# Optimization experiments

Hardware: AMD Instinct MI355X
Metric: run time of the kernel (lower is better)

## Reference

```python
import jax, jax.numpy as jnp
import numpy as np

VS = VT = 32000; E = 512; H = 512; B = 32; S = 128; T = 128


def _gru_step(x, h, Wx, bx, Urz, brz, Un, bn):
    # x: [B, I], h: [B, H]
    gx = x @ Wx + bx                       # [B, 3H]
    xr, xz, xn = jnp.split(gx, 3, axis=-1)
    hrz = h @ Urz + brz                    # [B, 2H]
    hr, hz = jnp.split(hrz, 2, axis=-1)
    r = jax.nn.sigmoid(xr + hr)
    z = jax.nn.sigmoid(xz + hz)
    n = jnp.tanh(xn + (r * h) @ Un + bn)
    return (1.0 - z) * h + z * n


def setup_inputs() -> dict:
    key = jax.random.key(0)
    ks = jax.random.split(key, 24)
    s = 0.02
    f = lambda k, shape: (jax.random.normal(k, shape, dtype=jnp.float32) * s)
    return {
        "src": jax.random.randint(ks[0], (B, S), 0, VS),
        "tgt": jax.random.randint(ks[1], (B, T), 0, VT),
        "enc_embed": f(ks[2], (VS, E)),
        "enc_Wx": f(ks[3], (E, 3 * H)),
        "enc_bx": jnp.zeros((3 * H,), jnp.float32),
        "enc_Urz": f(ks[4], (H, 2 * H)),
        "enc_brz": jnp.zeros((2 * H,), jnp.float32),
        "enc_Un": f(ks[5], (H, H)),
        "enc_bn": jnp.zeros((H,), jnp.float32),
        "dec_embed": f(ks[6], (VT, E)),
        "dec_Wx": f(ks[7], (E + H, 3 * H)),
        "dec_bx": jnp.zeros((3 * H,), jnp.float32),
        "dec_Urz": f(ks[8], (H, 2 * H)),
        "dec_brz": jnp.zeros((2 * H,), jnp.float32),
        "dec_Un": f(ks[9], (H, H)),
        "dec_bn": jnp.zeros((H,), jnp.float32),
        "attn_Wh": f(ks[10], (H, H)),
        "attn_Ws": f(ks[11], (H, H)),
        "attn_v": f(ks[12], (H,)),
        "out_W": f(ks[13], (2 * H, VT)),
        "out_b": jnp.zeros((VT,), jnp.float32),
    }


def reference(src, tgt, enc_embed, enc_Wx, enc_bx, enc_Urz, enc_brz, enc_Un,
              enc_bn, dec_embed, dec_Wx, dec_bx, dec_Urz, dec_brz, dec_Un,
              dec_bn, attn_Wh, attn_Ws, attn_v, out_W, out_b):
    bs = src.shape[0]
    h0 = jnp.zeros((bs, H), dtype=enc_Wx.dtype)

    # -------- encoder: scan over src timesteps --------
    src_emb = enc_embed[src]                     # [B, S, E]

    def enc_step(h, x_t):
        h = _gru_step(x_t, h, enc_Wx, enc_bx, enc_Urz, enc_brz, enc_Un, enc_bn)
        return h, h

    h, enc_hs = jax.lax.scan(enc_step, h0, jnp.swapaxes(src_emb, 0, 1))
    enc_hs = jnp.swapaxes(enc_hs, 0, 1)          # [B, S, H]

    # precompute Wh(enc_hs), identical every decoder step
    wh_enc = enc_hs @ attn_Wh                    # [B, S, H]

    # -------- decoder: scan over tgt timesteps --------
    tgt_emb = dec_embed[tgt]                     # [B, T, E]

    def dec_step(h, emb_t):
        # Bahdanau attention
        energy = jnp.einsum('bsh,h->bs', jnp.tanh(wh_enc + (h @ attn_Ws)[:, None, :]), attn_v)
        attn = jax.nn.softmax(energy, axis=-1)   # [B, S]
        ctx = jnp.einsum('bs,bsh->bh', attn, enc_hs)
        x = jnp.concatenate([emb_t, ctx], axis=-1)   # [B, E+H]
        h = _gru_step(x, h, dec_Wx, dec_bx, dec_Urz, dec_brz, dec_Un, dec_bn)
        logits = jnp.concatenate([h, ctx], axis=-1) @ out_W + out_b
        out = jax.nn.log_softmax(logits, axis=-1)
        return h, out

    _, outputs = jax.lax.scan(dec_step, h, jnp.swapaxes(tgt_emb, 0, 1))
    return jnp.swapaxes(outputs, 0, 1)           # [B, T, VT]
```

## Files before the change

kernel.cpp:

```cpp
#include <hip/hip_runtime.h>
#include <stdint.h>

#define BATCH 32
#define SEQ   128
#define HID   512
#define VTOK  32000

typedef unsigned short u16;
typedef unsigned int   u32;
typedef unsigned long long u64;
typedef float    f32x4  __attribute__((ext_vector_type(4)));
typedef short    short8 __attribute__((ext_vector_type(8)));

__device__ __forceinline__ u16 f2bf(float f) {
    u32 u = __builtin_bit_cast(u32, f);
    return (u16)((u + 0x7FFFu + ((u >> 16) & 1u)) >> 16);
}
__device__ __forceinline__ float bf2f(u16 v) {
    u32 u = ((u32)v) << 16; return __builtin_bit_cast(float, u);
}
__device__ __forceinline__ float fexp2(float x) { return __builtin_amdgcn_exp2f(x); }
__device__ __forceinline__ float frcp(float x)  { return __builtin_amdgcn_rcpf(x); }
__device__ __forceinline__ float sigmoid_f(float x) {
    return frcp(1.f + fexp2(-1.442695040888963f * x));
}
__device__ __forceinline__ float tanh_f(float x) {
    return 1.f - 2.f * frcp(1.f + fexp2(2.885390081777927f * x));
}

__device__ __forceinline__ u32 ld_sc1_u32(const u32* p) {
    return __hip_atomic_load(p, __ATOMIC_RELAXED, __HIP_MEMORY_SCOPE_AGENT);
}
__device__ __forceinline__ void st_sc1_u32(u32* p, u32 v) {
    __hip_atomic_store(p, v, __ATOMIC_RELAXED, __HIP_MEMORY_SCOPE_AGENT);
}
__device__ __forceinline__ u64 ld_sc1_u64(const u64* p) {
    return __hip_atomic_load(p, __ATOMIC_RELAXED, __HIP_MEMORY_SCOPE_AGENT);
}
__device__ __forceinline__ short8 ldA(const u64* base) {
    union { u64 q[2]; short8 s; } u;
    u.q[0] = ld_sc1_u64(base);
    u.q[1] = ld_sc1_u64(base + 1);
    return u.s;
}

__device__ __forceinline__ void gbar(u32* flags, u32 gen, int nwg) {
    asm volatile("s_waitcnt vmcnt(0)" ::: "memory");
    __syncthreads();
    if (threadIdx.x == 0) st_sc1_u32(flags + (u32)blockIdx.x * 16, gen);
    const int i = threadIdx.x;
    if (i < nwg && i != (int)blockIdx.x) {
        while (ld_sc1_u32(flags + i * 16) < gen) {}
    }
    __syncthreads();
}


__global__ __launch_bounds__(256) void transpose_cvt(
    const float* __restrict__ src, u16* __restrict__ dst, int K, int N)
{
    __shared__ float tile[32][33];
    const int n0 = blockIdx.x * 32, k0 = blockIdx.y * 32;
    const int tx = threadIdx.x & 31, ty = threadIdx.x >> 5;
    #pragma unroll
    for (int j = 0; j < 32; j += 8)
        tile[ty + j][tx] = src[(size_t)(k0 + ty + j) * N + n0 + tx];
    __syncthreads();
    #pragma unroll
    for (int j = 0; j < 32; j += 8)
        dst[(size_t)(n0 + ty + j) * K + k0 + tx] = f2bf(tile[tx][ty + j]);
}

__global__ __launch_bounds__(256) void cvt_f32_bf16(
    const float* __restrict__ src, u16* __restrict__ dst)
{
    const size_t i = ((size_t)blockIdx.x * 256 + threadIdx.x) * 8;
    float4 v0 = *(const float4*)(src + i);
    float4 v1 = *(const float4*)(src + i + 4);
    uint4 pk;
    pk.x = (u32)f2bf(v0.x) | ((u32)f2bf(v0.y) << 16);
    pk.y = (u32)f2bf(v0.z) | ((u32)f2bf(v0.w) << 16);
    pk.z = (u32)f2bf(v1.x) | ((u32)f2bf(v1.y) << 16);
    pk.w = (u32)f2bf(v1.z) | ((u32)f2bf(v1.w) << 16);
    *(uint4*)(dst + i) = pk;
}

__global__ __launch_bounds__(128) void gather_emb_bf16(
    const int* __restrict__ idx, const float* __restrict__ emb, u16* __restrict__ out)
{
    const int r = blockIdx.x;
    const int token = idx[r];
    const int i = threadIdx.x * 4;
    float4 v = *(const float4*)(emb + (size_t)token * 512 + i);
    uint2 pk;
    pk.x = (u32)f2bf(v.x) | ((u32)f2bf(v.y) << 16);
    pk.y = (u32)f2bf(v.z) | ((u32)f2bf(v.w) << 16);
    *(uint2*)(out + (size_t)r * 512 + i) = pk;
}

__global__ __launch_bounds__(512) void init_state(u32* hg, u32* bar)
{
    const int i = blockIdx.x * 512 + threadIdx.x;
    hg[i] = 0u;
    if (blockIdx.x < 8) bar[blockIdx.x * 512 + threadIdx.x] = 0u;
}

__global__ __launch_bounds__(256) void gemm_bf16(
    const u16* __restrict__ A, const u16* __restrict__ BT,
    const float* __restrict__ bias, float* __restrict__ C,
    int M, int N, int K)
{
    __shared__ __align__(16) u16 As[128][40];
    __shared__ __align__(16) u16 Bs[128][40];
    const int tid  = threadIdx.x;
    const int lane = tid & 63, wave = tid >> 6;
    const int wm = (wave & 1) * 64, wn = (wave >> 1) * 64;
    const int lrow = lane & 15, lk = (lane >> 4) * 8;
    const int srow = tid >> 2, skof = (tid & 3) * 8;
    const size_t K_ = (size_t)K;
    const u16* Ag = A + ((size_t)blockIdx.y * 128 + srow) * K_ + skof;
    const u16* Bg = BT + ((size_t)blockIdx.x * 128 + srow) * K_ + skof;
    f32x4 acc[4][4] = {};
    for (int k0 = 0; k0 < K; k0 += 32) {
        uint4 a0 = *(const uint4*)(Ag + k0);
        uint4 a1 = *(const uint4*)(Ag + 64 * K_ + k0);
        uint4 b0 = *(const uint4*)(Bg + k0);
        uint4 b1 = *(const uint4*)(Bg + 64 * K_ + k0);
        __syncthreads();
        *(uint4*)&As[srow][skof]      = a0;
        *(uint4*)&As[srow + 64][skof] = a1;
        *(uint4*)&Bs[srow][skof]      = b0;
        *(uint4*)&Bs[srow + 64][skof] = b1;
        __syncthreads();
        short8 af[4], bf[4];
        #pragma unroll
        for (int i = 0; i < 4; ++i) af[i] = *(const short8*)&As[wm + i * 16 + lrow][lk];
        #pragma unroll
        for (int j = 0; j < 4; ++j) bf[j] = *(const short8*)&Bs[wn + j * 16 + lrow][lk];
        #pragma unroll
        for (int i = 0; i < 4; ++i)
            #pragma unroll
            for (int j = 0; j < 4; ++j)
                acc[i][j] = __builtin_amdgcn_mfma_f32_16x16x32_bf16(af[i], bf[j], acc[i][j], 0, 0, 0);
    }
    const int crow0 = blockIdx.y * 128 + wm + (lane >> 4) * 4;
    const int ccol0 = blockIdx.x * 128 + wn + (lane & 15);
    #pragma unroll
    for (int j = 0; j < 4; ++j) {
        const float bv = bias ? bias[ccol0 + j * 16] : 0.f;
        #pragma unroll
        for (int i = 0; i < 4; ++i)
            #pragma unroll
            for (int rr = 0; rr < 4; ++rr)
                C[(size_t)(crow0 + i * 16 + rr) * N + (ccol0 + j * 16)] = acc[i][j][rr] + bv;
    }
}

__global__ __launch_bounds__(512) void enc_coop(
    const float* __restrict__ gx, const u16* __restrict__ Urz, const u16* __restrict__ Un,
    const float* __restrict__ brz, const float* __restrict__ bn,
    u32* __restrict__ hg, u32* __restrict__ rhg, u32* __restrict__ zg,
    u16* __restrict__ enc_hs, u16* __restrict__ spack,
    u32* __restrict__ flags)
{
    const int w = blockIdx.x, tid = threadIdx.x;
    const int v = tid >> 6, lane = tid & 63;
    const int nl = lane & 15, kq = lane >> 4;
    const u64* hq = (const u64*)hg;
    const u64* rq = (const u64*)rhg;
    u32 gen = 0u;
    for (int t = 0; t < SEQ; ++t) {
        if (v < 2) {
            const int bt = v;
            const int n = w * 16 + nl;
            const int brow = bt * 16 + nl;
            float gxr_pf[4]; u32 hv_pf[4];
            #pragma unroll
            for (int rr = 0; rr < 4; ++rr) {
                const int b = bt * 16 + kq * 4 + rr;
                gxr_pf[rr] = gx[((size_t)(b * SEQ + t)) * 1536 + n];
                if (n < 512) hv_pf[rr] = ld_sc1_u32(hg + b * 256 + (n >> 1));
            }
            const u16* wp = Urz + (size_t)n * 512 + kq * 8;
            f32x4 acc = {0.f, 0.f, 0.f, 0.f};
            #pragma unroll
            for (int k0 = 0; k0 < 512; k0 += 32) {
                short8 af = ldA(hq + brow * 128 + (k0 >> 2) + kq * 2);
                short8 bf = *(const short8*)(wp + k0);
                acc = __builtin_amdgcn_mfma_f32_16x16x32_bf16(af, bf, acc, 0, 0, 0);
            }
            if (n < 512) {
                u32 pk[4];
                #pragma unroll
                for (int rr = 0; rr < 4; ++rr) {
                    const float r = sigmoid_f(gxr_pf[rr] + acc[rr] + brz[n]);
                    const float hold = bf2f((u16)((n & 1) ? (hv_pf[rr] >> 16) : (hv_pf[rr] & 0xFFFF)));
                    pk[rr] = (u32)f2bf(r * hold);
                }
                #pragma unroll
                for (int rr = 0; rr < 4; ++rr) {
                    u32 oth = (u32)__shfl_xor((int)pk[rr], 1);
                    if ((n & 1) == 0) {
                        const int b = bt * 16 + kq * 4 + rr;
                        st_sc1_u32(rhg + b * 256 + (n >> 1), (pk[rr] & 0xFFFF) | (oth << 16));
                    }
                }
            } else {
                #pragma unroll
                for (int rr = 0; rr < 4; ++rr) {
                    const int b = bt * 16 + kq * 4 + rr;
                    const float z = sigmoid_f(gxr_pf[rr] + acc[rr] + brz[n]);
                    st_sc1_u32(zg + (n - 512) * 32 + b, __float_as_uint(z));
                }
            }
        }
        gbar(flags, ++gen, 64);
        if (v < 2 && w < 32) {
            const int bt = v;
            const int n = w * 16 + nl;
            const int brow = bt * 16 + nl;
            float gxr_pf[4]; u32 hv_pf[4], zv_pf[4];
            #pragma unroll
            for (int rr = 0; rr < 4; ++rr) {
                const int b = bt * 16 + kq * 4 + rr;
                gxr_pf[rr] = gx[((size_t)(b * SEQ + t)) * 1536 + 1024 + n];
                hv_pf[rr] = ld_sc1_u32(hg + b * 256 + (n >> 1));
                zv_pf[rr] = ld_sc1_u32(zg + n * 32 + b);
            }
            const u16* wp = Un + (size_t)n * 512 + kq * 8;
            f32x4 acc = {0.f, 0.f, 0.f, 0.f};
            #pragma unroll
            for (int k0 = 0; k0 < 512; k0 += 32) {
                short8 af = ldA(rq + brow * 128 + (k0 >> 2) + kq * 2);
                short8 bf = *(const short8*)(wp + k0);
                acc = __builtin_amdgcn_mfma_f32_16x16x32_bf16(af, bf, acc, 0, 0, 0);
            }
            u32 pk[4];
            #pragma unroll
            for (int rr = 0; rr < 4; ++rr) {
                const int b = bt * 16 + kq * 4 + rr;
                const float nn = tanh_f(gxr_pf[rr] + acc[rr] + bn[n]);
                const float z = __uint_as_float(zv_pf[rr]);
                const float hold = bf2f((u16)((n & 1) ? (hv_pf[rr] >> 16) : (hv_pf[rr] & 0xFFFF)));
                const float hn = (1.f - z) * hold + z * nn;
                const u16 hb = f2bf(hn);
                pk[rr] = (u32)hb;
                enc_hs[((size_t)(b * SEQ + t)) * 512 + n] = hb;
                spack[(((size_t)b * 16 + (t >> 3)) * 512 + n) * 8 + (t & 7)] = hb;
            }
            #pragma unroll
            for (int rr = 0; rr < 4; ++rr) {
                u32 oth = (u32)__shfl_xor((int)pk[rr], 1);
                if ((n & 1) == 0) {
                    const int b = bt * 16 + kq * 4 + rr;
                    st_sc1_u32(hg + b * 256 + (n >> 1), (pk[rr] & 0xFFFF) | (oth << 16));
                }
            }
        }
        gbar(flags, ++gen, 64);
    }
}

__global__ __launch_bounds__(512) void dec_coop(
    const float* __restrict__ gxe, const u16* __restrict__ wh_bf, const u16* __restrict__ spack,
    const float* __restrict__ attn_v, const float* __restrict__ brz, const float* __restrict__ bn,
    const u16* __restrict__ Urz, const u16* __restrict__ Ws,
    const u16* __restrict__ WxC, const u16* __restrict__ Un,
    u32* __restrict__ hg, u32* __restrict__ rhg, u32* __restrict__ ctxg,
    u32* __restrict__ zg, u32* __restrict__ gg, u32* __restrict__ aWsg,
    u16* __restrict__ hctx, u32* __restrict__ flags)
{
    const int w = blockIdx.x, tid = threadIdx.x;
    const int v = tid >> 6, lane = tid & 63;
    const int nl = lane & 15, kq = lane >> 4;
    __shared__ float hWsL[4 * 132], redE[512], attnL[128];
    __shared__ u16 ctxL[512];
    const u64* hq = (const u64*)hg;
    const u64* rq = (const u64*)rhg;
    const u64* cq = (const u64*)ctxg;
    u32 gen = 0u;
    for (int t = 0; t < SEQ; ++t) {
        f32x4 aPk = {0.f, 0.f, 0.f, 0.f};
        if (v < 2) {
            const int bt = v;
            const int n = w * 16 + nl;
            const int brow = bt * 16 + nl;
            const u16* wp = (n < 1024 ? Urz + (size_t)n * 512
                                      : Ws + (size_t)(n - 1024) * 512) + kq * 8;
            f32x4 acc = {0.f, 0.f, 0.f, 0.f};
            #pragma unroll
            for (int k0 = 0; k0 < 512; k0 += 32) {
                short8 af = ldA(hq + brow * 128 + (k0 >> 2) + kq * 2);
                short8 bf = *(const short8*)(wp + k0);
                acc = __builtin_amdgcn_mfma_f32_16x16x32_bf16(af, bf, acc, 0, 0, 0);
            }
            if (n < 1024) {
                aPk = acc;
            } else {
                #pragma unroll
                for (int rr = 0; rr < 4; ++rr) {
                    const int b = bt * 16 + kq * 4 + rr;
                    st_sc1_u32(aWsg + (n - 1024) * 32 + b, __float_as_uint(acc[rr]));
                }
            }
        }
        gbar(flags, ++gen, 96);
        if (w < 32) {
            const int b = w;
            hWsL[(tid >> 7) * 132 + (tid & 127)] = __uint_as_float(ld_sc1_u32(aWsg + tid * 32 + b));
            __syncthreads();
            {
                const int s = tid >> 2, q = tid & 3;
                const u16* whr = wh_bf + ((size_t)(b * SEQ + s)) * 512 + q * 128;
                const float* avq = attn_v + q * 128;
                const float* hwq = &hWsL[q * 132];
                float e = 0.f;
                #pragma unroll 4
                for (int i = 0; i < 128; i += 8) {
                    uint4 wv = *(const uint4*)(whr + i);
                    float4 h0 = *(const float4*)(hwq + i);
                    float4 h1 = *(const float4*)(hwq + i + 4);
                    float4 v0 = *(const float4*)(avq + i);
                    float4 v1 = *(const float4*)(avq + i + 4);
                    e += v0.x * tanh_f(bf2f((u16)(wv.x & 0xFFFF)) + h0.x)
                       + v0.y * tanh_f(bf2f((u16)(wv.x >> 16))    + h0.y)
                       + v0.z * tanh_f(bf2f((u16)(wv.y & 0xFFFF)) + h0.z)
                       + v0.w * tanh_f(bf2f((u16)(wv.y >> 16))    + h0.w)
                       + v1.x * tanh_f(bf2f((u16)(wv.z & 0xFFFF)) + h1.x)
                       + v1.y * tanh_f(bf2f((u16)(wv.z >> 16))    + h1.y)
                       + v1.z * tanh_f(bf2f((u16)(wv.w & 0xFFFF)) + h1.z)
                       + v1.w * tanh_f(bf2f((u16)(wv.w >> 16))    + h1.w);
                }
                redE[tid] = e;
            }
            __syncthreads();
            if (tid < 64) {
                float e0 = redE[4 * tid] + redE[4 * tid + 1] + redE[4 * tid + 2] + redE[4 * tid + 3];
                float e1 = redE[4 * (tid + 64)] + redE[4 * (tid + 64) + 1]
                         + redE[4 * (tid + 64) + 2] + redE[4 * (tid + 64) + 3];
                float m = fmaxf(e0, e1);
                for (int o = 32; o >= 1; o >>= 1) m = fmaxf(m, __shfl_xor(m, o));
                float p0 = fexp2((e0 - m) * 1.442695040888963f);
                float p1 = fexp2((e1 - m) * 1.442695040888963f);
                float ss = p0 + p1;
                for (int o = 32; o >= 1; o >>= 1) ss += __shfl_xor(ss, o);
                const float inv = frcp(ss);
                attnL[tid]      = p0 * inv;
                attnL[tid + 64] = p1 * inv;
            }
            __syncthreads();
            {
                const int d = tid;
                float cv = 0.f;
                const u16* sp = spack + ((size_t)b * 16 * 512 + d) * 8;
                #pragma unroll 4
                for (int sb = 0; sb < 16; ++sb) {
                    uint4 sv = *(const uint4*)(sp + (size_t)sb * 4096);
                    const float* al = &attnL[sb * 8];
                    cv += al[0] * bf2f((u16)(sv.x & 0xFFFF)) + al[1] * bf2f((u16)(sv.x >> 16))
                        + al[2] * bf2f((u16)(sv.y & 0xFFFF)) + al[3] * bf2f((u16)(sv.y >> 16))
                        + al[4] * bf2f((u16)(sv.z & 0xFFFF)) + al[5] * bf2f((u16)(sv.z >> 16))
                        + al[6] * bf2f((u16)(sv.w & 0xFFFF)) + al[7] * bf2f((u16)(sv.w >> 16));
                }
                const u16 cb = f2bf(cv);
                ctxL[d] = cb;
                hctx[((size_t)(b * SEQ + t)) * 1024 + 512 + d] = cb;
            }
            __syncthreads();
            if (tid < 256) {
                u32 pk = (u32)ctxL[2 * tid] | ((u32)ctxL[2 * tid + 1] << 16);
                st_sc1_u32(ctxg + b * 256 + tid, pk);
            }
        }
        gbar(flags, ++gen, 96);
        if (v < 2) {
            const int bt = v;
            const int n = w * 16 + nl;
            const int brow = bt * 16 + nl;
            float gxr_pf[4]; u32 hv_pf[4];
            #pragma unroll
            for (int rr = 0; rr < 4; ++rr) {
                const int b = bt * 16 + kq * 4 + rr;
                gxr_pf[rr] = gxe[((size_t)(b * SEQ + t)) * 1536 + n];
                if (n < 512) hv_pf[rr] = ld_sc1_u32(hg + b * 256 + (n >> 1));
            }
            const u16* wp = WxC + (size_t)n * 512 + kq * 8;
            f32x4 acc = {0.f, 0.f, 0.f, 0.f};
            #pragma unroll
            for (int k0 = 0; k0 < 512; k0 += 32) {
                short8 af = ldA(cq + brow * 128 + (k0 >> 2) + kq * 2);
                short8 bf = *(const short8*)(wp + k0);
                acc = __builtin_amdgcn_mfma_f32_16x16x32_bf16(af, bf, acc, 0, 0, 0);
            }
            if (n < 512) {
                u32 pk[4];
                #pragma unroll
                for (int rr = 0; rr < 4; ++rr) {
                    const float r = sigmoid_f(gxr_pf[rr] + acc[rr] + aPk[rr] + brz[n]);
                    const float hold = bf2f((u16)((n & 1) ? (hv_pf[rr] >> 16) : (hv_pf[rr] & 0xFFFF)));
                    pk[rr] = (u32)f2bf(r * hold);
                }
                #pragma unroll
                for (int rr = 0; rr < 4; ++rr) {
                    u32 oth = (u32)__shfl_xor((int)pk[rr], 1);
                    if ((n & 1) == 0) {
                        const int b = bt * 16 + kq * 4 + rr;
                        st_sc1_u32(rhg + b * 256 + (n >> 1), (pk[rr] & 0xFFFF) | (oth << 16));
                    }
                }
            } else if (n < 1024) {
                #pragma unroll
                for (int rr = 0; rr < 4; ++rr) {
                    const int b = bt * 16 + kq * 4 + rr;
                    const float z = sigmoid_f(gxr_pf[rr] + acc[rr] + aPk[rr] + brz[n]);
                    st_sc1_u32(zg + (n - 512) * 32 + b, __float_as_uint(z));
                }
            } else {
                #pragma unroll
                for (int rr = 0; rr < 4; ++rr) {
                    const int b = bt * 16 + kq * 4 + rr;
                    st_sc1_u32(gg + (n - 1024) * 32 + b, __float_as_uint(gxr_pf[rr] + acc[rr]));
                }
            }
        }
        gbar(flags, ++gen, 96);
        if (v < 2 && w < 32) {
            const int bt = v;
            const int n = w * 16 + nl;
            const int brow = bt * 16 + nl;
            u32 gv_pf[4], zv_pf[4], hv_pf[4];
            #pragma unroll
            for (int rr = 0; rr < 4; ++rr) {
                const int b = bt * 16 + kq * 4 + rr;
                gv_pf[rr] = ld_sc1_u32(gg + n * 32 + b);
                zv_pf[rr] = ld_sc1_u32(zg + n * 32 + b);
                hv_pf[rr] = ld_sc1_u32(hg + b * 256 + (n >> 1));
            }
            const u16* wp = Un + (size_t)n * 512 + kq * 8;
            f32x4 acc = {0.f, 0.f, 0.f, 0.f};
            #pragma unroll
            for (int k0 = 0; k0 < 512; k0 += 32) {
                short8 af = ldA(rq + brow * 128 + (k0 >> 2) + kq * 2);
                short8 bf = *(const short8*)(wp + k0);
                acc = __builtin_amdgcn_mfma_f32_16x16x32_bf16(af, bf, acc, 0, 0, 0);
            }
            u32 pk[4];
            #pragma unroll
            for (int rr = 0; rr < 4; ++rr) {
                const int b = bt * 16 + kq * 4 + rr;
                const float nn = tanh_f(__uint_as_float(gv_pf[rr]) + acc[rr] + bn[n]);
                const float z = __uint_as_float(zv_pf[rr]);
                const float hold = bf2f((u16)((n & 1) ? (hv_pf[rr] >> 16) : (hv_pf[rr] & 0xFFFF)));
                const float hn = (1.f - z) * hold + z * nn;
                const u16 hb = f2bf(hn);
                pk[rr] = (u32)hb;
                hctx[((size_t)(b * SEQ + t)) * 1024 + n] = hb;
            }
            #pragma unroll
            for (int rr = 0; rr < 4; ++rr) {
                u32 oth = (u32)__shfl_xor((int)pk[rr], 1);
                if ((n & 1) == 0) {
                    const int b = bt * 16 + kq * 4 + rr;
                    st_sc1_u32(hg + b * 256 + (n >> 1), (pk[rr] & 0xFFFF) | (oth << 16));
                }
            }
        }
        gbar(flags, ++gen, 96);
    }
}

__global__ __launch_bounds__(256) void log_softmax_rows(float* __restrict__ out)
{
    const int row = blockIdx.x, tid = threadIdx.x;
    float* p = out + (size_t)row * VTOK;
    __shared__ float rbM[4], rbS[4];
    const float L2E = 1.442695040888963f;
    float m = -3.0e38f, s = 0.f;
    for (int i = tid * 4; i < VTOK; i += 1024) {
        float4 v = *(const float4*)(p + i);
        float lm = fmaxf(fmaxf(v.x, v.y), fmaxf(v.z, v.w));
        float nm = fmaxf(m, lm);
        s = s * fexp2((m - nm) * L2E)
          + fexp2((v.x - nm) * L2E) + fexp2((v.y - nm) * L2E)
          + fexp2((v.z - nm) * L2E) + fexp2((v.w - nm) * L2E);
        m = nm;
    }
    for (int o = 32; o >= 1; o >>= 1) {
        float om = __shfl_xor(m, o), os = __shfl_xor(s, o);
        float nm = fmaxf(m, om);
        s = s * fexp2((m - nm) * L2E) + os * fexp2((om - nm) * L2E);
        m = nm;
    }
    if ((tid & 63) == 0) { rbM[tid >> 6] = m; rbS[tid >> 6] = s; }
    __syncthreads();
    {
        float fm = fmaxf(fmaxf(rbM[0], rbM[1]), fmaxf(rbM[2], rbM[3]));
        float fs = rbS[0] * fexp2((rbM[0] - fm) * L2E) + rbS[1] * fexp2((rbM[1] - fm) * L2E)
                 + rbS[2] * fexp2((rbM[2] - fm) * L2E) + rbS[3] * fexp2((rbM[3] - fm) * L2E);
        m = fm; s = fs;
    }
    const float lse = m + __builtin_amdgcn_logf(s) * 0.6931471805599453f;
    for (int i = tid * 4; i < VTOK; i += 1024) {
        float4 v = *(const float4*)(p + i);
        v.x -= lse; v.y -= lse; v.z -= lse; v.w -= lse;
        *(float4*)(p + i) = v;
    }
}

extern "C" void kernel_launch(void* const* d_in, const int* in_sizes, int n_in,
                              void* d_out, int out_size, void* d_ws, size_t ws_size,
                              hipStream_t stream)
{
    (void)in_sizes; (void)n_in; (void)out_size; (void)ws_size;
    const int*   src       = (const int*)  d_in[0];
    const int*   tgt       = (const int*)  d_in[1];
    const float* enc_embed = (const float*)d_in[2];
    const float* enc_Wx    = (const float*)d_in[3];
    const float* enc_bx    = (const float*)d_in[4];
    const float* enc_Urz   = (const float*)d_in[5];
    const float* enc_brz   = (const float*)d_in[6];
    const float* enc_Un    = (const float*)d_in[7];
    const float* enc_bn    = (const float*)d_in[8];
    const float* dec_embed = (const float*)d_in[9];
    const float* dec_Wx    = (const float*)d_in[10];
    const float* dec_bx    = (const float*)d_in[11];
    const float* dec_Urz   = (const float*)d_in[12];
    const float* dec_brz   = (const float*)d_in[13];
    const float* dec_Un    = (const float*)d_in[14];
    const float* dec_bn    = (const float*)d_in[15];
    const float* attn_Wh   = (const float*)d_in[16];
    const float* attn_Ws   = (const float*)d_in[17];
    const float* attn_v    = (const float*)d_in[18];
    const float* out_W     = (const float*)d_in[19];
    const float* out_b     = (const float*)d_in[20];

    char* ob = (char*)d_out;
    float* gx_enc   = (float*)(ob + 0);
    float* gxe_dec  = (float*)(ob + 25165824);
    float* wh_enc   = (float*)(ob + 50331648);
    u16*   Aenc     = (u16*)(ob + 58720256);
    u16*   Adec     = (u16*)(ob + 62914560);
    u16*   enc_hs   = (u16*)(ob + 67108864);
    u16*   spack    = (u16*)(ob + 71303168);
    u16*   wh_bf    = (u16*)(ob + 75497472);
    u16*   encWxT   = (u16*)(ob + 79691776);
    u16*   decWxET  = (u16*)(ob + 81264640);
    u16*   WhT      = (u16*)(ob + 82837504);
    u16*   UrzET    = (u16*)(ob + 83361792);
    u16*   UnET     = (u16*)(ob + 84410368);
    u16*   UrzDT    = (u16*)(ob + 84934656);
    u16*   UnDT     = (u16*)(ob + 85983232);
    u16*   WsT      = (u16*)(ob + 86507520);
    u16*   WxCT     = (u16*)(ob + 87031808);
    u32*   hg       = (u32*)(ob + 88604672);
    u32*   rhg      = (u32*)(ob + 88637440);
    u32*   ctxg     = (u32*)(ob + 88670208);
    u32*   zg       = (u32*)(ob + 88702976);
    u32*   gg       = (u32*)(ob + 88768512);
    u32*   aWsg     = (u32*)(ob + 88834048);
    u32*   barp     = (u32*)(ob + 88899584);

    char* wb = (char*)d_ws;
    u16* outWT = (u16*)(wb + 0);
    u16* hctx  = (u16*)(wb + 65536000);

    transpose_cvt<<<dim3(48, 16),   256, 0, stream>>>(enc_Wx,  encWxT, 512, 1536);
    transpose_cvt<<<dim3(48, 16),   256, 0, stream>>>(dec_Wx,  decWxET,512, 1536);
    transpose_cvt<<<dim3(16, 16),   256, 0, stream>>>(attn_Wh, WhT,    512, 512);
    transpose_cvt<<<dim3(1000, 32), 256, 0, stream>>>(out_W,   outWT, 1024, 32000);
    transpose_cvt<<<dim3(32, 16),   256, 0, stream>>>(enc_Urz, UrzET,  512, 1024);
    transpose_cvt<<<dim3(16, 16),   256, 0, stream>>>(enc_Un,  UnET,   512, 512);
    transpose_cvt<<<dim3(32, 16),   256, 0, stream>>>(dec_Urz, UrzDT,  512, 1024);
    transpose_cvt<<<dim3(16, 16),   256, 0, stream>>>(dec_Un,  UnDT,   512, 512);
    transpose_cvt<<<dim3(16, 16),   256, 0, stream>>>(attn_Ws, WsT,    512, 512);
    transpose_cvt<<<dim3(48, 16),   256, 0, stream>>>(dec_Wx + (size_t)512 * 1536, WxCT, 512, 1536);
    gather_emb_bf16<<<4096, 128, 0, stream>>>(src, enc_embed, Aenc);
    gather_emb_bf16<<<4096, 128, 0, stream>>>(tgt, dec_embed, Adec);

    gemm_bf16<<<dim3(12, 32), 256, 0, stream>>>(Aenc, encWxT,  enc_bx, gx_enc,  4096, 1536, 512);
    gemm_bf16<<<dim3(12, 32), 256, 0, stream>>>(Adec, decWxET, dec_bx, gxe_dec, 4096, 1536, 512);

    init_state<<<16, 512, 0, stream>>>(hg, barp);

    {
        u32* encF = barp;
        void* args[] = { (void*)&gx_enc, (void*)&UrzET, (void*)&UnET, (void*)&enc_brz,
                         (void*)&enc_bn, (void*)&hg, (void*)&rhg, (void*)&zg,
                         (void*)&enc_hs, (void*)&spack, (void*)&encF };
        hipLaunchCooperativeKernel((void*)enc_coop, dim3(64), dim3(512), args, 0, stream);
    }

    gemm_bf16<<<dim3(4, 32), 256, 0, stream>>>(enc_hs, WhT, nullptr, wh_enc, 4096, 512, 512);
    cvt_f32_bf16<<<1024, 256, 0, stream>>>(wh_enc, wh_bf);

    {
        u32* decF = barp + 1024;
        void* args[] = { (void*)&gxe_dec, (void*)&wh_bf, (void*)&spack, (void*)&attn_v,
                         (void*)&dec_brz, (void*)&dec_bn, (void*)&UrzDT, (void*)&WsT,
                         (void*)&WxCT, (void*)&UnDT, (void*)&hg, (void*)&rhg, (void*)&ctxg,
                         (void*)&zg, (void*)&gg, (void*)&aWsg, (void*)&hctx, (void*)&decF };
        hipLaunchCooperativeKernel((void*)dec_coop, dim3(96), dim3(512), args, 0, stream);
    }

    gemm_bf16<<<dim3(250, 32), 256, 0, stream>>>(hctx, outWT, out_b, (float*)d_out, 4096, VTOK, 1024);
    log_softmax_rows<<<4096, 256, 0, stream>>>((float*)d_out);
}
```

Baseline: 6.429 ms.

## Replace all-to-all grid barriers with targeted flag waits and double-buffered hidden state

The full grid barriers in the encoder and decoder cooperative kernels are replaced with per-workgroup generation flags. Each phase now waits only on the producer workgroups it actually depends on, for example the first 32 for h or the specific attention and gate workgroups. The hidden state is double-buffered by timestep parity, which removes write-after-read hazards and lets workgroups finish their end-of-step signal without a second rendezvous. This cuts barrier latency on the serial recurrence. The cost is more complex dependency reasoning, and a missed dependency could cause silent races.

```diff
diff --git a/kernel.cpp b/kernel.cpp
--- a/kernel.cpp
+++ b/kernel.cpp
@@ -44,15 +44,14 @@
     return u.s;
 }
 
-__device__ __forceinline__ void gbar(u32* flags, u32 gen, int nwg) {
+__device__ __forceinline__ void poll_ge(const u32* f, int idx, u32 gen) {
+    const u32* p = f + (u32)idx * 16;
+    while (ld_sc1_u32(p) < gen) {}
+}
+__device__ __forceinline__ void bump(u32* f, u32 gen) {
     asm volatile("s_waitcnt vmcnt(0)" ::: "memory");
     __syncthreads();
-    if (threadIdx.x == 0) st_sc1_u32(flags + (u32)blockIdx.x * 16, gen);
-    const int i = threadIdx.x;
-    if (i < nwg && i != (int)blockIdx.x) {
-        while (ld_sc1_u32(flags + i * 16) < gen) {}
-    }
-    __syncthreads();
+    if (threadIdx.x == 0) st_sc1_u32(f + (u32)blockIdx.x * 16, gen);
 }
 
 
@@ -102,7 +101,7 @@
 {
     const int i = blockIdx.x * 512 + threadIdx.x;
     hg[i] = 0u;
-    if (blockIdx.x < 8) bar[blockIdx.x * 512 + threadIdx.x] = 0u;
+    if (blockIdx.x < 6) bar[blockIdx.x * 512 + threadIdx.x] = 0u;
 }
 
 __global__ __launch_bounds__(256) void gemm_bf16(
@@ -166,10 +165,12 @@
     const int w = blockIdx.x, tid = threadIdx.x;
     const int v = tid >> 6, lane = tid & 63;
     const int nl = lane & 15, kq = lane >> 4;
-    const u64* hq = (const u64*)hg;
     const u64* rq = (const u64*)rhg;
-    u32 gen = 0u;
     for (int t = 0; t < SEQ; ++t) {
+        const u32* hgA = hg + (t & 1) * 8192;
+        u32*       hgW = hg + ((t + 1) & 1) * 8192;
+        const u64* hq  = (const u64*)hgA;
+        { if (tid < 32) poll_ge(flags, tid, (u32)(2 * t)); __syncthreads(); }
         if (v < 2) {
             const int bt = v;
             const int n = w * 16 + nl;
@@ -179,7 +180,7 @@
             for (int rr = 0; rr < 4; ++rr) {
                 const int b = bt * 16 + kq * 4 + rr;
                 gxr_pf[rr] = gx[((size_t)(b * SEQ + t)) * 1536 + n];
-                if (n < 512) hv_pf[rr] = ld_sc1_u32(hg + b * 256 + (n >> 1));
+                if (n < 512) hv_pf[rr] = ld_sc1_u32(hgA + b * 256 + (n >> 1));
             }
             const u16* wp = Urz + (size_t)n * 512 + kq * 8;
             f32x4 acc = {0.f, 0.f, 0.f, 0.f};
@@ -214,50 +215,53 @@
                 }
             }
         }
-        gbar(flags, ++gen, 64);
-        if (v < 2 && w < 32) {
-            const int bt = v;
-            const int n = w * 16 + nl;
-            const int brow = bt * 16 + nl;
-            float gxr_pf[4]; u32 hv_pf[4], zv_pf[4];
-            #pragma unroll
-            for (int rr = 0; rr < 4; ++rr) {
-                const int b = bt * 16 + kq * 4 + rr;
-                gxr_pf[rr] = gx[((size_t)(b * SEQ + t)) * 1536 + 1024 + n];
-                hv_pf[rr] = ld_sc1_u32(hg + b * 256 + (n >> 1));
-                zv_pf[rr] = ld_sc1_u32(zg + n * 32 + b);
-            }
-            const u16* wp = Un + (size_t)n * 512 + kq * 8;
-            f32x4 acc = {0.f, 0.f, 0.f, 0.f};
-            #pragma unroll
-            for (int k0 = 0; k0 < 512; k0 += 32) {
-                short8 af = ldA(rq + brow * 128 + (k0 >> 2) + kq * 2);
-                short8 bf = *(const short8*)(wp + k0);
-                acc = __builtin_amdgcn_mfma_f32_16x16x32_bf16(af, bf, acc, 0, 0, 0);
-            }
-            u32 pk[4];
-            #pragma unroll
-            for (int rr = 0; rr < 4; ++rr) {
-                const int b = bt * 16 + kq * 4 + rr;
-                const float nn = tanh_f(gxr_pf[rr] + acc[rr] + bn[n]);
-                const float z = __uint_as_float(zv_pf[rr]);
-                const float hold = bf2f((u16)((n & 1) ? (hv_pf[rr] >> 16) : (hv_pf[rr] & 0xFFFF)));
-                const float hn = (1.f - z) * hold + z * nn;
-                const u16 hb = f2bf(hn);
-                pk[rr] = (u32)hb;
-                enc_hs[((size_t)(b * SEQ + t)) * 512 + n] = hb;
-                spack[(((size_t)b * 16 + (t >> 3)) * 512 + n) * 8 + (t & 7)] = hb;
-            }
-            #pragma unroll
-            for (int rr = 0; rr < 4; ++rr) {
-                u32 oth = (u32)__shfl_xor((int)pk[rr], 1);
-                if ((n & 1) == 0) {
-                    const int b = bt * 16 + kq * 4 + rr;
-                    st_sc1_u32(hg + b * 256 + (n >> 1), (pk[rr] & 0xFFFF) | (oth << 16));
+        bump(flags, (u32)(2 * t + 1));
+        if (w < 32) {
+            { if (tid < 64) poll_ge(flags, tid, (u32)(2 * t + 1)); __syncthreads(); }
+            if (v < 2) {
+                const int bt = v;
+                const int n = w * 16 + nl;
+                const int brow = bt * 16 + nl;
+                float gxr_pf[4]; u32 hv_pf[4], zv_pf[4];
+                #pragma unroll
+                for (int rr = 0; rr < 4; ++rr) {
+                    const int b = bt * 16 + kq * 4 + rr;
+                    gxr_pf[rr] = gx[((size_t)(b * SEQ + t)) * 1536 + 1024 + n];
+                    hv_pf[rr] = ld_sc1_u32(hgA + b * 256 + (n >> 1));
+                    zv_pf[rr] = ld_sc1_u32(zg + n * 32 + b);
+                }
+                const u16* wp = Un + (size_t)n * 512 + kq * 8;
+                f32x4 acc = {0.f, 0.f, 0.f, 0.f};
+                #pragma unroll
+                for (int k0 = 0; k0 < 512; k0 += 32) {
+                    short8 af = ldA(rq + brow * 128 + (k0 >> 2) + kq * 2);
+                    short8 bf = *(const short8*)(wp + k0);
+                    acc = __builtin_amdgcn_mfma_f32_16x16x32_bf16(af, bf, acc, 0, 0, 0);
+                }
+                u32 pk[4];
+                #pragma unroll
+                for (int rr = 0; rr < 4; ++rr) {
+                    const int b = bt * 16 + kq * 4 + rr;
+                    const float nn = tanh_f(gxr_pf[rr] + acc[rr] + bn[n]);
+                    const float z = __uint_as_float(zv_pf[rr]);
+                    const float hold = bf2f((u16)((n & 1) ? (hv_pf[rr] >> 16) : (hv_pf[rr] & 0xFFFF)));
+                    const float hn = (1.f - z) * hold + z * nn;
+                    const u16 hb = f2bf(hn);
+                    pk[rr] = (u32)hb;
+                    enc_hs[((size_t)(b * SEQ + t)) * 512 + n] = hb;
+                    spack[(((size_t)b * 16 + (t >> 3)) * 512 + n) * 8 + (t & 7)] = hb;
+                }
+                #pragma unroll
+                for (int rr = 0; rr < 4; ++rr) {
+                    u32 oth = (u32)__shfl_xor((int)pk[rr], 1);
+                    if ((n & 1) == 0) {
+                        const int b = bt * 16 + kq * 4 + rr;
+                        st_sc1_u32(hgW + b * 256 + (n >> 1), (pk[rr] & 0xFFFF) | (oth << 16));
+                    }
                 }
             }
         }
-        gbar(flags, ++gen, 64);
+        bump(flags, (u32)(2 * t + 2));
     }
 }
 
@@ -275,12 +279,14 @@
     const int nl = lane & 15, kq = lane >> 4;
     __shared__ float hWsL[4 * 132], redE[512], attnL[128];
     __shared__ u16 ctxL[512];
-    const u64* hq = (const u64*)hg;
     const u64* rq = (const u64*)rhg;
     const u64* cq = (const u64*)ctxg;
-    u32 gen = 0u;
     for (int t = 0; t < SEQ; ++t) {
+        const u32* hgA = hg + (t & 1) * 8192;
+        u32*       hgW = hg + ((t + 1) & 1) * 8192;
+        const u64* hq  = (const u64*)hgA;
         f32x4 aPk = {0.f, 0.f, 0.f, 0.f};
+        { if (tid < 32) poll_ge(flags, tid, (u32)(4 * t)); __syncthreads(); }
         if (v < 2) {
             const int bt = v;
             const int n = w * 16 + nl;
@@ -304,8 +310,17 @@
                 }
             }
         }
-        gbar(flags, ++gen, 96);
+        bump(flags, (u32)(4 * t + 1));
         if (w < 32) {
+            {
+                const int l = tid;
+                if (l < 96) {
+                    int g0 = 4 * t - 1; if (g0 < 0) g0 = 0;
+                    u32 g = (l >= 64) ? (u32)(4 * t + 1) : (u32)g0;
+                    poll_ge(flags, l, g);
+                }
+                __syncthreads();
+            }
             const int b = w;
             hWsL[(tid >> 7) * 132 + (tid & 127)] = __uint_as_float(ld_sc1_u32(aWsg + tid * 32 + b));
             __syncthreads();
@@ -372,7 +387,8 @@
                 st_sc1_u32(ctxg + b * 256 + tid, pk);
             }
         }
-        gbar(flags, ++gen, 96);
+        bump(flags, (u32)(4 * t + 2));
+        { if (tid < 32) poll_ge(flags, tid, (u32)(4 * t + 2)); __syncthreads(); }
         if (v < 2) {
             const int bt = v;
             const int n = w * 16 + nl;
@@ -382,7 +398,7 @@
             for (int rr = 0; rr < 4; ++rr) {
                 const int b = bt * 16 + kq * 4 + rr;
                 gxr_pf[rr] = gxe[((size_t)(b * SEQ + t)) * 1536 + n];
-                if (n < 512) hv_pf[rr] = ld_sc1_u32(hg + b * 256 + (n >> 1));
+                if (n < 512) hv_pf[rr] = ld_sc1_u32(hgA + b * 256 + (n >> 1));
             }
             const u16* wp = WxC + (size_t)n * 512 + kq * 8;
             f32x4 acc = {0.f, 0.f, 0.f, 0.f};
@@ -423,49 +439,58 @@
                 }
             }
         }
-        gbar(flags, ++gen, 96);
-        if (v < 2 && w < 32) {
-            const int bt = v;
-            const int n = w * 16 + nl;
-            const int brow = bt * 16 + nl;
-            u32 gv_pf[4], zv_pf[4], hv_pf[4];
-            #pragma unroll
-            for (int rr = 0; rr < 4; ++rr) {
-                const int b = bt * 16 + kq * 4 + rr;
-                gv_pf[rr] = ld_sc1_u32(gg + n * 32 + b);
-                zv_pf[rr] = ld_sc1_u32(zg + n * 32 + b);
-                hv_pf[rr] = ld_sc1_u32(hg + b * 256 + (n >> 1));
-            }
-            const u16* wp = Un + (size_t)n * 512 + kq * 8;
-            f32x4 acc = {0.f, 0.f, 0.f, 0.f};
-            #pragma unroll
-            for (int k0 = 0; k0 < 512; k0 += 32) {
-                short8 af = ldA(rq + brow * 128 + (k0 >> 2) + kq * 2);
-                short8 bf = *(const short8*)(wp + k0);
-                acc = __builtin_amdgcn_mfma_f32_16x16x32_bf16(af, bf, acc, 0, 0, 0);
-            }
-            u32 pk[4];
-            #pragma unroll
-            for (int rr = 0; rr < 4; ++rr) {
-                const int b = bt * 16 + kq * 4 + rr;
-                const float nn = tanh_f(__uint_as_float(gv_pf[rr]) + acc[rr] + bn[n]);
-                const float z = __uint_as_float(zv_pf[rr]);
-                const float hold = bf2f((u16)((n & 1) ? (hv_pf[rr] >> 16) : (hv_pf[rr] & 0xFFFF)));
-                const float hn = (1.f - z) * hold + z * nn;
-                const u16 hb = f2bf(hn);
-                pk[rr] = (u32)hb;
-                hctx[((size_t)(b * SEQ + t)) * 1024 + n] = hb;
-            }
-            #pragma unroll
-            for (int rr = 0; rr < 4; ++rr) {
-                u32 oth = (u32)__shfl_xor((int)pk[rr], 1);
-                if ((n & 1) == 0) {
-                    const int b = bt * 16 + kq * 4 + rr;
-                    st_sc1_u32(hg + b * 256 + (n >> 1), (pk[rr] & 0xFFFF) | (oth << 16));
+        bump(flags, (u32)(4 * t + 3));
+        if (w < 32) {
+            {
+                const int l = tid;
+                if (l < 32) poll_ge(flags, l, (u32)(4 * t + 3));
+                else if (l == 32) poll_ge(flags, 32 + w, (u32)(4 * t + 3));
+                else if (l == 33) poll_ge(flags, 64 + w, (u32)(4 * t + 3));
+                __syncthreads();
+            }
+            if (v < 2) {
+                const int bt = v;
+                const int n = w * 16 + nl;
+                const int brow = bt * 16 + nl;
+                u32 gv_pf[4], zv_pf[4], hv_pf[4];
+                #pragma unroll
+                for (int rr = 0; rr < 4; ++rr) {
+                    const int b = bt * 16 + kq * 4 + rr;
+                    gv_pf[rr] = ld_sc1_u32(gg + n * 32 + b);
+                    zv_pf[rr] = ld_sc1_u32(zg + n * 32 + b);
+                    hv_pf[rr] = ld_sc1_u32(hgA + b * 256 + (n >> 1));
+                }
+                const u16* wp = Un + (size_t)n * 512 + kq * 8;
+                f32x4 acc = {0.f, 0.f, 0.f, 0.f};
+                #pragma unroll
+                for (int k0 = 0; k0 < 512; k0 += 32) {
+                    short8 af = ldA(rq + brow * 128 + (k0 >> 2) + kq * 2);
+                    short8 bf = *(const short8*)(wp + k0);
+                    acc = __builtin_amdgcn_mfma_f32_16x16x32_bf16(af, bf, acc, 0, 0, 0);
+                }
+                u32 pk[4];
+                #pragma unroll
+                for (int rr = 0; rr < 4; ++rr) {
+                    const int b = bt * 16 + kq * 4 + rr;
+                    const float nn = tanh_f(__uint_as_float(gv_pf[rr]) + acc[rr] + bn[n]);
+                    const float z = __uint_as_float(zv_pf[rr]);
+                    const float hold = bf2f((u16)((n & 1) ? (hv_pf[rr] >> 16) : (hv_pf[rr] & 0xFFFF)));
+                    const float hn = (1.f - z) * hold + z * nn;
+                    const u16 hb = f2bf(hn);
+                    pk[rr] = (u32)hb;
+                    hctx[((size_t)(b * SEQ + t)) * 1024 + n] = hb;
+                }
+                #pragma unroll
+                for (int rr = 0; rr < 4; ++rr) {
+                    u32 oth = (u32)__shfl_xor((int)pk[rr], 1);
+                    if ((n & 1) == 0) {
+                        const int b = bt * 16 + kq * 4 + rr;
+                        st_sc1_u32(hgW + b * 256 + (n >> 1), (pk[rr] & 0xFFFF) | (oth << 16));
+                    }
                 }
             }
         }
-        gbar(flags, ++gen, 96);
+        bump(flags, (u32)(4 * t + 4));
     }
 }
 
@@ -553,12 +578,12 @@
     u16*   WsT      = (u16*)(ob + 86507520);
     u16*   WxCT     = (u16*)(ob + 87031808);
     u32*   hg       = (u32*)(ob + 88604672);
-    u32*   rhg      = (u32*)(ob + 88637440);
-    u32*   ctxg     = (u32*)(ob + 88670208);
-    u32*   zg       = (u32*)(ob + 88702976);
-    u32*   gg       = (u32*)(ob + 88768512);
-    u32*   aWsg     = (u32*)(ob + 88834048);
-    u32*   barp     = (u32*)(ob + 88899584);
+    u32*   rhg      = (u32*)(ob + 88670208);
+    u32*   ctxg     = (u32*)(ob + 88702976);
+    u32*   zg       = (u32*)(ob + 88735744);
+    u32*   gg       = (u32*)(ob + 88801280);
+    u32*   aWsg     = (u32*)(ob + 88866816);
+    u32*   barp     = (u32*)(ob + 88932352);
 
     char* wb = (char*)d_ws;
     u16* outWT = (u16*)(wb + 0);
@@ -580,7 +605,7 @@
     gemm_bf16<<<dim3(12, 32), 256, 0, stream>>>(Aenc, encWxT,  enc_bx, gx_enc,  4096, 1536, 512);
     gemm_bf16<<<dim3(12, 32), 256, 0, stream>>>(Adec, decWxET, dec_bx, gxe_dec, 4096, 1536, 512);
 
-    init_state<<<16, 512, 0, stream>>>(hg, barp);
+    init_state<<<32, 512, 0, stream>>>(hg, barp);
 
     {
         u32* encF = barp;
@@ -594,7 +619,7 @@
     cvt_f32_bf16<<<1024, 256, 0, stream>>>(wh_enc, wh_bf);
 
     {
-        u32* decF = barp + 1024;
+        u32* decF = barp + 1536;
         void* args[] = { (void*)&gxe_dec, (void*)&wh_bf, (void*)&spack, (void*)&attn_v,
                          (void*)&dec_brz, (void*)&dec_bn, (void*)&UrzDT, (void*)&WsT,
                          (void*)&WxCT, (void*)&UnDT, (void*)&hg, (void*)&rhg, (void*)&ctxg,
```

Result: no change. 6.397 ms (-0.5%).
